# Performance work log

Measured on AMD Instinct MI355X. Metric: run time of the kernel, lower is better.

The kernel has to match this reference:

```python
import jax, jax.numpy as jnp
import numpy as np

N = 200000          # active input voxels
GRID = 96           # voxel grid extent
_OFFS = np.array([[dx, dy, dz] for dx in (-1, 0, 1) for dy in (-1, 0, 1) for dz in (-1, 0, 1)], dtype=np.int64)  # 27 kernel offsets


def _build_kmap(cin, cout, stride):
    """Build gather/scatter kernel maps for a 3x3x3 sparse conv.
    For each offset k and each output j, find input i with coord_in[i] == coord_out[j]*stride + off[k].
    Misses scatter to sentinel row n_out (dropped) and gather row 0 (value ignored)."""
    B = int(max(cin.max(), cout.max() * stride + 1)) + 3
    key_in = (cin[:, 0].astype(np.int64) * B + cin[:, 1]) * B + cin[:, 2]
    order = np.argsort(key_in).astype(np.int32)
    sk = key_in[order]
    n_out = cout.shape[0]
    g = np.zeros((27, n_out), np.int32)
    s = np.full((27, n_out), n_out, np.int32)
    ar = np.arange(n_out, dtype=np.int32)
    co = cout.astype(np.int64)
    for k in range(27):
        q = co * stride + _OFFS[k]
        valid = (q >= 0).all(axis=1)
        qk = (q[:, 0] * B + q[:, 1]) * B + q[:, 2]
        pos = np.clip(np.searchsorted(sk, qk), 0, sk.shape[0] - 1)
        found = valid & (sk[pos] == qk)
        g[k] = np.where(found, order[pos], 0)
        s[k] = np.where(found, ar, n_out)
    return jnp.asarray(g), jnp.asarray(s)


def setup_inputs() -> dict:
    rng = np.random.RandomState(0)
    raw = rng.randint(0, GRID, size=(3 * N, 3))
    coords = np.unique(raw, axis=0)[:N]          # [N,3] unique voxel coords
    c1 = coords
    c2 = np.unique(c1 // 2, axis=0)              # stride-2 output coords
    g1, s1 = _build_kmap(c1, c1, 1)              # submanifold conv1
    g2, s2 = _build_kmap(c1, c2, 2)              # strided conv2
    g3, s3 = _build_kmap(c2, c2, 1)              # submanifold conv3
    key = jax.random.key(0)
    k1, k2, k3, k4 = jax.random.split(key, 4)
    feats = jax.random.normal(k1, (N, 4), jnp.float32)
    W1 = jax.random.normal(k2, (27, 4, 32), jnp.float32) * (1.0 / np.sqrt(27 * 4))
    W2 = jax.random.normal(k3, (27, 32, 32), jnp.float32) * (1.0 / np.sqrt(27 * 32))
    W3 = jax.random.normal(k4, (27, 32, 2), jnp.float32) * (1.0 / np.sqrt(27 * 32))
    return {"feats": feats, "W1": W1, "W2": W2, "W3": W3,
            "g1": g1, "s1": s1, "g2": g2, "s2": s2, "g3": g3, "s3": s3}


def _sparse_conv(feats, W, gidx, sidx):
    n_out = sidx.shape[1]
    c_out = W.shape[-1]
    gathered = feats[gidx]                              # [27, M, Cin] irregular gather
    contrib = jnp.einsum('kmc,kcd->kmd', gathered, W)   # per-offset GEMM
    out = jnp.zeros((n_out + 1, c_out), feats.dtype)    # +1 sentinel row for misses
    out = out.at[sidx.reshape(-1)].add(contrib.reshape(-1, c_out))  # scatter-add
    return out[:n_out]


def reference(feats, W1, W2, W3, g1, s1, g2, s2, g3, s3):
    x = _sparse_conv(feats, W1, g1, s1)
    x = _sparse_conv(x, W2, g2, s2)
    x = _sparse_conv(x, W3, g3, s3)
    return x
```

## Files before the change

### kernel.cpp

```cpp
#include <hip/hip_runtime.h>

#define CDIV(a,b) (((a)+(b)-1)/(b))

typedef __attribute__((ext_vector_type(8)))  short short8v;
typedef __attribute__((ext_vector_type(4)))  short short4v;
typedef __attribute__((ext_vector_type(16))) float f32x16;

__device__ inline unsigned short f2bf(float x) {
    unsigned u = __builtin_bit_cast(unsigned, x);
    u += 0x7fffu + ((u >> 16) & 1u);
    return (unsigned short)(u >> 16);
}

__global__ __launch_bounds__(256) void prep_k(
    const float* __restrict__ feats, const float* __restrict__ W1,
    const float* __restrict__ W2, const float* __restrict__ W3,
    unsigned short* __restrict__ featsh, unsigned short* __restrict__ x1h,
    unsigned short* __restrict__ x2h,
    unsigned short* __restrict__ w1p, unsigned short* __restrict__ w2p,
    unsigned short* __restrict__ w3p, int N, int M)
{
    int i = blockIdx.x * 256 + threadIdx.x;
    if (i < N) {
        float4 f = *reinterpret_cast<const float4*>(feats + (size_t)i * 4);
        ushort4 h; h.x = f2bf(f.x); h.y = f2bf(f.y); h.z = f2bf(f.z); h.w = f2bf(f.w);
        *reinterpret_cast<ushort4*>(featsh + (size_t)i * 4) = h;
        return;
    }
    if (i == N) {
        *reinterpret_cast<ushort4*>(featsh + (size_t)N * 4) = make_ushort4(0, 0, 0, 0);
        #pragma unroll
        for (int t = 0; t < 8; ++t) {
            *reinterpret_cast<ushort4*>(x1h + (size_t)N * 32 + t * 4) = make_ushort4(0, 0, 0, 0);
            *reinterpret_cast<ushort4*>(x2h + (size_t)M * 32 + t * 4) = make_ushort4(0, 0, 0, 0);
        }
        return;
    }
    int j = i - (N + 1);
    if (j < 4096) {
        int m = j >> 9, t = j & 511, l = t >> 3, e = t & 7;
        int h = l >> 5, r = l & 31;
        int kk = h * 8 + e, slot = 4 * m + (kk >> 2), c = kk & 3;
        float v = (slot < 27) ? W1[slot * 128 + c * 32 + r] : 0.f;
        w1p[j] = f2bf(v);
        return;
    }
    j -= 4096;
    if (j < 27 * 1024) {
        int k = j >> 10, idx = j & 1023, p = idx >> 9, t = idx & 511;
        int l = t >> 3, e = t & 7, h = l >> 5, r = l & 31;
        int c = p * 16 + h * 8 + e;
        w2p[j] = f2bf(W2[k * 1024 + c * 32 + r]);
        return;
    }
    j -= 27 * 1024;
    if (j < 27 * 1024) {
        int k = j >> 10, idx = j & 1023, p = idx >> 9, t = idx & 511;
        int l = t >> 3, e = t & 7, h = l >> 5, r = l & 31;
        int c = p * 16 + h * 8 + e;
        float v = (r < 2) ? W3[k * 64 + c * 2 + r] : 0.f;
        w3p[j] = f2bf(v);
    }
}

__global__ __launch_bounds__(256) void conv1_k(
    const unsigned short* __restrict__ featsh, const unsigned short* __restrict__ w1p,
    const int* __restrict__ g1, const int* __restrict__ s1,
    unsigned short* __restrict__ x1h, int N)
{
    int tid = threadIdx.x;
    int l = tid & 63, wv = tid >> 6;
    int r = l & 31, h = l >> 5;
    int rbase = blockIdx.x * 128 + wv * 32;
    int j = rbase + r;
    int jc = j < N ? j : N - 1;

    int gm[8][2];
    #pragma unroll
    for (int m = 0; m < 8; ++m)
        #pragma unroll
        for (int t = 0; t < 2; ++t) {
            int slot = 4 * m + 2 * h + t;
            int v = N;
            if (slot < 27 && j < N) {
                int s = s1[(size_t)slot * N + jc];
                int g = g1[(size_t)slot * N + jc];
                v = (s != N) ? g : N;
            }
            gm[m][t] = v;
        }

    f32x16 acc = {};
    const char* fb = (const char*)featsh;
    const char* wb = (const char*)w1p;
    #pragma unroll
    for (int m = 0; m < 8; ++m) {
        short4v lo = *(const short4v*)(fb + (size_t)gm[m][0] * 8);
        short4v hi = *(const short4v*)(fb + (size_t)gm[m][1] * 8);
        short8v a = __builtin_shufflevector(lo, hi, 0, 1, 2, 3, 4, 5, 6, 7);
        short8v b = *(const short8v*)(wb + m * 1024 + l * 16);
        acc = __builtin_amdgcn_mfma_f32_32x32x16_bf16(a, b, acc, 0, 0, 0);
    }
    #pragma unroll
    for (int reg = 0; reg < 16; ++reg) {
        int row = (reg & 3) + 8 * (reg >> 2) + 4 * h;
        int j2 = rbase + row;
        if (j2 < N) x1h[(size_t)j2 * 32 + r] = f2bf(acc[reg]);
    }
}

__global__ __launch_bounds__(256) void conv2_k(
    const unsigned short* __restrict__ x1h, const unsigned short* __restrict__ w2p,
    const int* __restrict__ g2, const int* __restrict__ s2,
    unsigned short* __restrict__ x2h, int M, int N)
{
    int tid = threadIdx.x;
    int l = tid & 63, wv = tid >> 6;
    int r = l & 31, h = l >> 5;
    int rbase = blockIdx.x * 128 + wv * 32;
    int j = rbase + r;
    int jc = j < M ? j : M - 1;

    int gm[27];
    #pragma unroll
    for (int k = 0; k < 27; ++k) {
        int s = s2[(size_t)k * M + jc];
        int g = g2[(size_t)k * M + jc];
        gm[k] = (j < M && s != M) ? g : N;
    }

    f32x16 acc = {};
    const char* xb = (const char*)x1h;
    const char* wb = (const char*)w2p;
    #pragma unroll
    for (int k = 0; k < 27; ++k) {
        const char* xr = xb + (size_t)gm[k] * 64;
        short8v a0 = *(const short8v*)(xr + h * 16);
        short8v a1 = *(const short8v*)(xr + 32 + h * 16);
        short8v b0 = *(const short8v*)(wb + k * 2048 + l * 16);
        short8v b1 = *(const short8v*)(wb + k * 2048 + 1024 + l * 16);
        acc = __builtin_amdgcn_mfma_f32_32x32x16_bf16(a0, b0, acc, 0, 0, 0);
        acc = __builtin_amdgcn_mfma_f32_32x32x16_bf16(a1, b1, acc, 0, 0, 0);
    }
    #pragma unroll
    for (int reg = 0; reg < 16; ++reg) {
        int row = (reg & 3) + 8 * (reg >> 2) + 4 * h;
        int j2 = rbase + row;
        if (j2 < M) x2h[(size_t)j2 * 32 + r] = f2bf(acc[reg]);
    }
}

__global__ __launch_bounds__(256) void conv3_k(
    const unsigned short* __restrict__ x2h, const unsigned short* __restrict__ w3p,
    const int* __restrict__ g3, const int* __restrict__ s3,
    float* __restrict__ out, int M)
{
    int tid = threadIdx.x;
    int l = tid & 63, wv = tid >> 6;
    int r = l & 31, h = l >> 5;
    int rbase = blockIdx.x * 128 + wv * 32;
    int j = rbase + r;
    int jc = j < M ? j : M - 1;

    int gm[27];
    #pragma unroll
    for (int k = 0; k < 27; ++k) {
        int s = s3[(size_t)k * M + jc];
        int g = g3[(size_t)k * M + jc];
        gm[k] = (j < M && s != M) ? g : M;
    }

    f32x16 acc = {};
    const char* xb = (const char*)x2h;
    const char* wb = (const char*)w3p;
    #pragma unroll
    for (int k = 0; k < 27; ++k) {
        const char* xr = xb + (size_t)gm[k] * 64;
        short8v a0 = *(const short8v*)(xr + h * 16);
        short8v a1 = *(const short8v*)(xr + 32 + h * 16);
        short8v b0 = *(const short8v*)(wb + k * 2048 + l * 16);
        short8v b1 = *(const short8v*)(wb + k * 2048 + 1024 + l * 16);
        acc = __builtin_amdgcn_mfma_f32_32x32x16_bf16(a0, b0, acc, 0, 0, 0);
        acc = __builtin_amdgcn_mfma_f32_32x32x16_bf16(a1, b1, acc, 0, 0, 0);
    }
    if (r < 2) {
        #pragma unroll
        for (int reg = 0; reg < 16; ++reg) {
            int row = (reg & 3) + 8 * (reg >> 2) + 4 * h;
            int j2 = rbase + row;
            if (j2 < M) out[(size_t)j2 * 2 + r] = acc[reg];
        }
    }
}

extern "C" void kernel_launch(void* const* d_in, const int* in_sizes, int n_in,
                              void* d_out, int out_size, void* d_ws, size_t ws_size,
                              hipStream_t stream) {
    const float* feats = (const float*)d_in[0];
    const float* W1    = (const float*)d_in[1];
    const float* W2    = (const float*)d_in[2];
    const float* W3    = (const float*)d_in[3];
    const int*   g1    = (const int*)d_in[4];
    const int*   s1    = (const int*)d_in[5];
    const int*   g2    = (const int*)d_in[6];
    const int*   s2    = (const int*)d_in[7];
    const int*   g3    = (const int*)d_in[8];
    const int*   s3    = (const int*)d_in[9];

    int N = in_sizes[0] / 4;
    int M = in_sizes[6] / 27;

    char* wsb = (char*)d_ws;
    size_t off = 0;
    auto alloc = [&](size_t bytes) {
        char* p = wsb + off;
        off = (off + bytes + 255) & ~(size_t)255;
        return p;
    };
    unsigned short* x1h    = (unsigned short*)alloc((size_t)(N + 1) * 64);
    unsigned short* x2h    = (unsigned short*)alloc((size_t)(M + 1) * 64);
    unsigned short* featsh = (unsigned short*)alloc((size_t)(N + 1) * 8);
    unsigned short* w1p    = (unsigned short*)alloc(4096 * 2);
    unsigned short* w2p    = (unsigned short*)alloc(27 * 1024 * 2);
    unsigned short* w3p    = (unsigned short*)alloc(27 * 1024 * 2);
    float* out = (float*)d_out;

    int prep_items = (N + 1) + 4096 + 27 * 1024 + 27 * 1024;
    prep_k<<<CDIV(prep_items, 256), 256, 0, stream>>>(
        feats, W1, W2, W3, featsh, x1h, x2h, w1p, w2p, w3p, N, M);
    conv1_k<<<CDIV(N, 128), 256, 0, stream>>>(featsh, w1p, g1, s1, x1h, N);
    conv2_k<<<CDIV(M, 128), 256, 0, stream>>>(x1h, w2p, g2, s2, x2h, M, N);
    conv3_k<<<CDIV(M, 128), 256, 0, stream>>>(x2h, w3p, g3, s3, out, M);
}
```

Measured before the change: 169.3 us.

## Fuse prep and three conv stages into one cooperative persistent kernel

Replaces four separate launches with a single cooperative kernel that runs the prep stage and each conv stage in turn, with grid.sync between stages. Within each stage, waves take 32-row units from an atomic work counter, so the grid is persistent and balances load dynamically. This removes inter-kernel launch gaps and tail effects. In exchange it adds grid-wide barrier cost and an occupancy query on every call, and it caps occupancy at the cooperative grid size, which could reduce the latency hiding available to the gathers. The old multi-kernel path stays as a fallback if the cooperative launch fails.

```diff
diff --git a/kernel.cpp b/kernel.cpp
--- a/kernel.cpp
+++ b/kernel.cpp
@@ -1,4 +1,7 @@
 #include <hip/hip_runtime.h>
+#include <hip/hip_cooperative_groups.h>
+
+namespace cg = cooperative_groups;
 
 #define CDIV(a,b) (((a)+(b)-1)/(b))
 
@@ -12,7 +15,8 @@
     return (unsigned short)(u >> 16);
 }
 
-__global__ __launch_bounds__(256) void prep_k(
+
+__device__ inline void prep_item(int i,
     const float* __restrict__ feats, const float* __restrict__ W1,
     const float* __restrict__ W2, const float* __restrict__ W3,
     unsigned short* __restrict__ featsh, unsigned short* __restrict__ x1h,
@@ -20,7 +24,6 @@
     unsigned short* __restrict__ w1p, unsigned short* __restrict__ w2p,
     unsigned short* __restrict__ w3p, int N, int M)
 {
-    int i = blockIdx.x * 256 + threadIdx.x;
     if (i < N) {
         float4 f = *reinterpret_cast<const float4*>(feats + (size_t)i * 4);
         ushort4 h; h.x = f2bf(f.x); h.y = f2bf(f.y); h.z = f2bf(f.z); h.w = f2bf(f.w);
@@ -63,15 +66,12 @@
     }
 }
 
-__global__ __launch_bounds__(256) void conv1_k(
+__device__ inline void conv1_unit(int rbase, int l,
     const unsigned short* __restrict__ featsh, const unsigned short* __restrict__ w1p,
     const int* __restrict__ g1, const int* __restrict__ s1,
     unsigned short* __restrict__ x1h, int N)
 {
-    int tid = threadIdx.x;
-    int l = tid & 63, wv = tid >> 6;
     int r = l & 31, h = l >> 5;
-    int rbase = blockIdx.x * 128 + wv * 32;
     int j = rbase + r;
     int jc = j < N ? j : N - 1;
 
@@ -109,15 +109,12 @@
     }
 }
 
-__global__ __launch_bounds__(256) void conv2_k(
+__device__ inline void conv2_unit(int rbase, int l,
     const unsigned short* __restrict__ x1h, const unsigned short* __restrict__ w2p,
     const int* __restrict__ g2, const int* __restrict__ s2,
     unsigned short* __restrict__ x2h, int M, int N)
 {
-    int tid = threadIdx.x;
-    int l = tid & 63, wv = tid >> 6;
     int r = l & 31, h = l >> 5;
-    int rbase = blockIdx.x * 128 + wv * 32;
     int j = rbase + r;
     int jc = j < M ? j : M - 1;
 
@@ -150,15 +147,12 @@
     }
 }
 
-__global__ __launch_bounds__(256) void conv3_k(
+__device__ inline void conv3_unit(int rbase, int l,
     const unsigned short* __restrict__ x2h, const unsigned short* __restrict__ w3p,
     const int* __restrict__ g3, const int* __restrict__ s3,
     float* __restrict__ out, int M)
 {
-    int tid = threadIdx.x;
-    int l = tid & 63, wv = tid >> 6;
     int r = l & 31, h = l >> 5;
-    int rbase = blockIdx.x * 128 + wv * 32;
     int j = rbase + r;
     int jc = j < M ? j : M - 1;
 
@@ -191,6 +185,110 @@
             if (j2 < M) out[(size_t)j2 * 2 + r] = acc[reg];
         }
     }
+}
+
+__global__ __launch_bounds__(256, 2) void fused_k(
+    const float* __restrict__ feats, const float* __restrict__ W1,
+    const float* __restrict__ W2, const float* __restrict__ W3,
+    const int* __restrict__ g1, const int* __restrict__ s1,
+    const int* __restrict__ g2, const int* __restrict__ s2,
+    const int* __restrict__ g3, const int* __restrict__ s3,
+    unsigned short* __restrict__ featsh, unsigned short* __restrict__ x1h,
+    unsigned short* __restrict__ x2h,
+    unsigned short* __restrict__ w1p, unsigned short* __restrict__ w2p,
+    unsigned short* __restrict__ w3p,
+    float* __restrict__ out, int* __restrict__ ctr, int N, int M)
+{
+    cg::grid_group grid = cg::this_grid();
+    int tid  = threadIdx.x;
+    int gtid = blockIdx.x * 256 + tid;
+    int lane = tid & 63;
+
+    if (gtid == 0) { atomicExch(&ctr[0], 0); atomicExch(&ctr[1], 0); atomicExch(&ctr[2], 0); }
+    int prep_items = (N + 1) + 4096 + 27 * 1024 + 27 * 1024;
+    int gstride = gridDim.x * 256;
+    for (int i = gtid; i < prep_items; i += gstride)
+        prep_item(i, feats, W1, W2, W3, featsh, x1h, x2h, w1p, w2p, w3p, N, M);
+    grid.sync();
+
+    {
+        int U = CDIV(N, 32);
+        int u;
+        if (lane == 0) u = atomicAdd(&ctr[0], 1);
+        u = __shfl(u, 0, 64);
+        while (u < U) {
+            conv1_unit(u * 32, lane, featsh, w1p, g1, s1, x1h, N);
+            if (lane == 0) u = atomicAdd(&ctr[0], 1);
+            u = __shfl(u, 0, 64);
+        }
+    }
+    grid.sync();
+
+    {
+        int U = CDIV(M, 32);
+        int u;
+        if (lane == 0) u = atomicAdd(&ctr[1], 1);
+        u = __shfl(u, 0, 64);
+        while (u < U) {
+            conv2_unit(u * 32, lane, x1h, w2p, g2, s2, x2h, M, N);
+            if (lane == 0) u = atomicAdd(&ctr[1], 1);
+            u = __shfl(u, 0, 64);
+        }
+    }
+    grid.sync();
+
+    {
+        int U = CDIV(M, 32);
+        int u;
+        if (lane == 0) u = atomicAdd(&ctr[2], 1);
+        u = __shfl(u, 0, 64);
+        while (u < U) {
+            conv3_unit(u * 32, lane, x2h, w3p, g3, s3, out, M);
+            if (lane == 0) u = atomicAdd(&ctr[2], 1);
+            u = __shfl(u, 0, 64);
+        }
+    }
+}
+
+__global__ __launch_bounds__(256) void prep_k(
+    const float* __restrict__ feats, const float* __restrict__ W1,
+    const float* __restrict__ W2, const float* __restrict__ W3,
+    unsigned short* __restrict__ featsh, unsigned short* __restrict__ x1h,
+    unsigned short* __restrict__ x2h,
+    unsigned short* __restrict__ w1p, unsigned short* __restrict__ w2p,
+    unsigned short* __restrict__ w3p, int N, int M)
+{
+    int i = blockIdx.x * 256 + threadIdx.x;
+    int items = (N + 1) + 4096 + 27 * 1024 + 27 * 1024;
+    if (i < items)
+        prep_item(i, feats, W1, W2, W3, featsh, x1h, x2h, w1p, w2p, w3p, N, M);
+}
+
+__global__ __launch_bounds__(256) void conv1_k(
+    const unsigned short* __restrict__ featsh, const unsigned short* __restrict__ w1p,
+    const int* __restrict__ g1, const int* __restrict__ s1,
+    unsigned short* __restrict__ x1h, int N)
+{
+    int tid = threadIdx.x;
+    conv1_unit(blockIdx.x * 128 + (tid >> 6) * 32, tid & 63, featsh, w1p, g1, s1, x1h, N);
+}
+
+__global__ __launch_bounds__(256) void conv2_k(
+    const unsigned short* __restrict__ x1h, const unsigned short* __restrict__ w2p,
+    const int* __restrict__ g2, const int* __restrict__ s2,
+    unsigned short* __restrict__ x2h, int M, int N)
+{
+    int tid = threadIdx.x;
+    conv2_unit(blockIdx.x * 128 + (tid >> 6) * 32, tid & 63, x1h, w2p, g2, s2, x2h, M, N);
+}
+
+__global__ __launch_bounds__(256) void conv3_k(
+    const unsigned short* __restrict__ x2h, const unsigned short* __restrict__ w3p,
+    const int* __restrict__ g3, const int* __restrict__ s3,
+    float* __restrict__ out, int M)
+{
+    int tid = threadIdx.x;
+    conv3_unit(blockIdx.x * 128 + (tid >> 6) * 32, tid & 63, x2h, w3p, g3, s3, out, M);
 }
 
 extern "C" void kernel_launch(void* const* d_in, const int* in_sizes, int n_in,
@@ -223,12 +321,32 @@
     unsigned short* w1p    = (unsigned short*)alloc(4096 * 2);
     unsigned short* w2p    = (unsigned short*)alloc(27 * 1024 * 2);
     unsigned short* w3p    = (unsigned short*)alloc(27 * 1024 * 2);
+    int*            ctr    = (int*)alloc(64);
     float* out = (float*)d_out;
 
-    int prep_items = (N + 1) + 4096 + 27 * 1024 + 27 * 1024;
-    prep_k<<<CDIV(prep_items, 256), 256, 0, stream>>>(
-        feats, W1, W2, W3, featsh, x1h, x2h, w1p, w2p, w3p, N, M);
-    conv1_k<<<CDIV(N, 128), 256, 0, stream>>>(featsh, w1p, g1, s1, x1h, N);
-    conv2_k<<<CDIV(M, 128), 256, 0, stream>>>(x1h, w2p, g2, s2, x2h, M, N);
-    conv3_k<<<CDIV(M, 128), 256, 0, stream>>>(x2h, w3p, g3, s3, out, M);
-}
+    int nb = 0;
+    hipError_t qe = hipOccupancyMaxActiveBlocksPerMultiprocessor(&nb, fused_k, 256, 0);
+    bool done = false;
+    if (qe == hipSuccess && nb > 0) {
+        int grid = 256 * nb;
+        if (grid > 2048) grid = 2048;
+        void* args[] = {
+            (void*)&feats, (void*)&W1, (void*)&W2, (void*)&W3,
+            (void*)&g1, (void*)&s1, (void*)&g2, (void*)&s2, (void*)&g3, (void*)&s3,
+            (void*)&featsh, (void*)&x1h, (void*)&x2h,
+            (void*)&w1p, (void*)&w2p, (void*)&w3p,
+            (void*)&out, (void*)&ctr, (void*)&N, (void*)&M };
+        hipError_t e = hipLaunchCooperativeKernel(fused_k, dim3(grid), dim3(256),
+                                                  args, 0, stream);
+        done = (e == hipSuccess);
+    }
+
+    if (!done) {
+        int prep_items = (N + 1) + 4096 + 27 * 1024 + 27 * 1024;
+        prep_k<<<CDIV(prep_items, 256), 256, 0, stream>>>(
+            feats, W1, W2, W3, featsh, x1h, x2h, w1p, w2p, w3p, N, M);
+        conv1_k<<<CDIV(N, 128), 256, 0, stream>>>(featsh, w1p, g1, s1, x1h, N);
+        conv2_k<<<CDIV(M, 128), 256, 0, stream>>>(x1h, w2p, g2, s2, x2h, M, N);
+        conv3_k<<<CDIV(M, 128), 256, 0, stream>>>(x2h, w3p, g3, s3, out, M);
+    }
+}
```

After: 167.2 us. Within noise of the previous version (-1.2%).
